# Kernel tuning notes

Hardware: AMD Instinct MI355X
Metric: run time of the kernel (lower is better)

The kernel has to match this reference:

```python
import jax, jax.numpy as jnp
import numpy as np

D = 128
N_ATOMS = 200000
E_ATOMS = 800000
G = 2000            # num molecule graphs = nDrug + nProtein
N_BIG = 7000        # nDrug + nProtein + nSe
E_BIG = 200000
N_EMB = 100001


def _edges(key, n, e):
    # random edges guaranteed to have no self-loops (PyG convs strip/re-add them)
    k1, k2 = jax.random.split(key)
    src = jax.random.randint(k1, (e,), 0, n)
    off = jax.random.randint(k2, (e,), 1, n)
    return jnp.stack([src, (src + off) % n])


def setup_inputs() -> dict:
    key = jax.random.key(0)
    ks = jax.random.split(key, 40)
    s = 0.09  # ~1/sqrt(D) init scale
    nrm = lambda i, shape: jax.random.normal(ks[i], shape, dtype=jnp.float32) * s
    inp = {}
    inp['x_ids'] = jax.random.randint(ks[0], (N_BIG,), 0, N_EMB)
    inp['drugEdges'] = _edges(ks[1], N_BIG, E_BIG)
    inp['seEdges'] = _edges(ks[2], 5000, 1000)  # unused by forward
    inp['drugNodes'] = jax.random.randint(ks[3], (1000,), 0, N_BIG)
    inp['seNodes'] = jax.random.randint(ks[4], (5000,), 0, N_BIG)
    inp['proteinNodes'] = jax.random.randint(ks[5], (1000,), 0, N_EMB)
    inp['proteinWeight'] = jax.random.normal(ks[6], (1000,), dtype=jnp.float32)
    inp['atom_x'] = jax.random.randint(ks[7], (N_ATOMS,), 0, N_EMB)
    inp['atom_edge_index'] = _edges(ks[8], N_ATOMS, E_ATOMS)
    inp['atom_batch'] = jnp.sort(jax.random.randint(ks[9], (N_ATOMS,), 0, G))
    inp['nDrug'] = 1000
    inp['emb'] = jax.random.uniform(ks[10], (N_EMB, D), minval=0.001, maxval=0.3, dtype=jnp.float32)
    for i in range(3):
        inp[f'gatW{i+1}'] = nrm(11 + i, (D, D))
        inp[f'attS{i+1}'] = nrm(14 + i, (D,))
        inp[f'attD{i+1}'] = nrm(17 + i, (D,))
        inp[f'gatB{i+1}'] = nrm(20 + i, (D,))
        inp[f'poolP{i+1}'] = nrm(23 + i, (D,))
    inp['lin1_W'] = nrm(26, (2 * D, D))
    inp['lin1_b'] = nrm(27, (D,))
    inp['gcn1_W'] = nrm(28, (D, D))
    inp['gcn1_b'] = nrm(29, (D,))
    inp['gcn2_W'] = nrm(30, (D, D))
    inp['gcn2_b'] = nrm(31, (D,))
    return inp


def _gat(x, src, dst, n, W, a_s, a_d, b):
    # PyG GATConv, 1 head: h = xW; e_ij = LeakyReLU(a_s.h_j + a_d.h_i);
    # softmax over incoming edges of i (self-loops re-added); out_i = sum_j alpha_ij h_j + b
    h = x @ W
    loops = jnp.arange(n)
    s = jnp.concatenate([src, loops])
    d = jnp.concatenate([dst, loops])
    e = jax.nn.leaky_relu((h @ a_s)[s] + (h @ a_d)[d], 0.2)
    m = jax.ops.segment_max(e, d, num_segments=n)
    ex = jnp.exp(e - m[d])
    z = jax.ops.segment_sum(ex, d, num_segments=n)
    w = ex / z[d]
    return jax.ops.segment_sum(w[:, None] * h[s], d, num_segments=n) + b


def _gcn(x, src, dst, n, W, b):
    loops = jnp.arange(n)
    s = jnp.concatenate([src, loops])
    d = jnp.concatenate([dst, loops])
    deg = jax.ops.segment_sum(jnp.ones(d.shape[0], x.dtype), d, num_segments=n)
    dis = deg ** -0.5
    coef = dis[s] * dis[d]
    return jax.ops.segment_sum(coef[:, None] * (x @ W)[s], d, num_segments=n) + b


def _topk1(x, p):
    # TopKPooling with ratio=1: keep all nodes, gate by tanh of projection score
    score = (x @ p) / jnp.linalg.norm(p)
    return x * jnp.tanh(score)[:, None]


def _gmp_gap(x, batch, g):
    mx = jax.ops.segment_max(x, batch, num_segments=g)
    sm = jax.ops.segment_sum(x, batch, num_segments=g)
    cnt = jax.ops.segment_sum(jnp.ones((x.shape[0], 1), x.dtype), batch, num_segments=g)
    return jnp.concatenate([mx, sm / jnp.maximum(cnt, 1.0)], axis=1)


def reference(x_ids, drugEdges, seEdges, drugNodes, seNodes, proteinNodes, proteinWeight,
              atom_x, atom_edge_index, atom_batch, nDrug, emb,
              gatW1, attS1, attD1, gatB1, poolP1,
              gatW2, attS2, attD2, gatB2, poolP2,
              gatW3, attS3, attD3, gatB3, poolP3,
              lin1_W, lin1_b, gcn1_W, gcn1_b, gcn2_W, gcn2_b):
    na = atom_x.shape[0]
    asrc, adst = atom_edge_index[0], atom_edge_index[1]
    xa = emb[atom_x]                                   # [na, D]
    xa = jax.nn.relu(_gat(xa, asrc, adst, na, gatW1, attS1, attD1, gatB1))
    xa = _topk1(xa, poolP1)
    x1 = _gmp_gap(xa, atom_batch, G)                   # [G, 2D]
    xa = jax.nn.relu(_gat(xa, asrc, adst, na, gatW2, attS2, attD2, gatB2))
    xa = _topk1(xa, poolP2)
    x2 = _gmp_gap(xa, atom_batch, G)
    xa = jax.nn.relu(_gat(xa, asrc, adst, na, gatW3, attS3, attD3, gatB3))
    xa = _topk1(xa, poolP3)
    x3 = _gmp_gap(xa, atom_batch, G)
    xDP = jax.nn.relu((x1 + x2 + x3) @ lin1_W + lin1_b)  # [G, D]
    nProtein = proteinNodes.shape[0]
    xse = emb[x_ids[nDrug + nProtein:]]                # side-effect node embeddings
    xb = jnp.concatenate([xDP, xse], axis=0)           # [N_BIG, D]
    dsrc, ddst = drugEdges[0], drugEdges[1]
    xb = jax.nn.relu(_gcn(xb, dsrc, ddst, N_BIG, gcn1_W, gcn1_b))
    xb = jax.nn.relu(_gcn(xb, dsrc, ddst, N_BIG, gcn2_W, gcn2_b))
    return (xb[drugNodes], xb[seNodes], xb)
```

## Files before the change

kernel.cpp:

```cpp
#include <hip/hip_runtime.h>
#include <cfloat>
#include <cmath>

#define D 128
#define N_ATOMS 200000
#define E_ATOMS 800000
#define G_GROUPS 2000
#define N_BIG 7000
#define E_BIG 200000
#define N_ALL (N_ATOMS + N_BIG)
#define E_ALL (E_ATOMS + E_BIG)

static inline int ceil_div(int a, int b) { return (a + b - 1) / b; }

typedef __attribute__((ext_vector_type(8))) _Float16 f16x8;
typedef __attribute__((ext_vector_type(2))) _Float16 h2_t;
typedef __attribute__((ext_vector_type(4))) float f32x4;

__device__ inline h2_t u2h(unsigned u) { return __builtin_bit_cast(h2_t, u); }
__device__ inline unsigned h2u(h2_t h) { return __builtin_bit_cast(unsigned, h); }
__device__ inline unsigned packh2(float x, float y) {
  h2_t h;
  h[0] = (_Float16)x;
  h[1] = (_Float16)y;
  return h2u(h);
}
__device__ inline float leaky(float e) { return fmaxf(e, 0.2f * e); }
__device__ inline float fast_tanh(float x) {
  float cx = fminf(fmaxf(x, -15.f), 15.f);
  float t = __expf(2.f * cx);
  return (t - 1.f) * __frcp_rn(t + 1.f);
}

__global__ void count_all(const int* __restrict__ adst, const int* __restrict__ ddst, int* __restrict__ deg,
                          int* __restrict__ rank) {
  int i = blockIdx.x * 256 + threadIdx.x;
  if (i < E_ATOMS)
    rank[i] = atomicAdd(&deg[adst[i]], 1);
  else if (i < E_ALL)
    rank[i] = atomicAdd(&deg[N_ATOMS + ddst[i - E_ATOMS]], 1);
}

__global__ void fill_csx(const int* __restrict__ asrc, const int* __restrict__ adst,
                         const int* __restrict__ dsrc, const int* __restrict__ ddst,
                         const int* __restrict__ rpx, const int* __restrict__ rank, int* __restrict__ csx) {
  int i = blockIdx.x * 256 + threadIdx.x;
  if (i < E_ATOMS) {
    csx[rpx[adst[i]] + rank[i]] = asrc[i];
  } else if (i < E_ALL) {
    int k = i - E_ATOMS;
    csx[rpx[N_ATOMS + ddst[k]] + rank[i]] = dsrc[k];
  }
}

__global__ void fill_pad(const int* __restrict__ deg, const int* __restrict__ rpx, int* __restrict__ csx) {
  int d = blockIdx.x * 256 + threadIdx.x;
  if (d >= N_ALL) return;
  int dg = deg[d];
  int b = rpx[d], e = rpx[d + 1];
  int sv = (d < N_ATOMS) ? d : d - N_ATOMS;
  for (int j = b + dg; j < e; ++j) csx[j] = sv;
}

__global__ void post_count(const int* __restrict__ deg, int* __restrict__ cntp, float* __restrict__ dis) {
  int i = blockIdx.x * 256 + threadIdx.x;
  if (i < N_ALL) cntp[i] = (deg[i] + 8) & ~7;
  if (i < N_BIG) dis[i] = 1.f / sqrtf((float)(deg[N_ATOMS + i] + 1));
}

__global__ __launch_bounds__(256) void scan_phase1(const int* __restrict__ in, int* __restrict__ out,
                                                   int* __restrict__ bsums, int n) {
  __shared__ int lds[256];
  int t = threadIdx.x;
  int base = blockIdx.x * 1024;
  int v[4];
  int s = 0;
#pragma unroll
  for (int j = 0; j < 4; ++j) {
    int i = base + t * 4 + j;
    v[j] = (i < n) ? in[i] : 0;
    s += v[j];
  }
  lds[t] = s;
  __syncthreads();
  for (int off = 1; off < 256; off <<= 1) {
    int x = (t >= off) ? lds[t - off] : 0;
    __syncthreads();
    lds[t] += x;
    __syncthreads();
  }
  int excl = lds[t] - s;
  if (t == 255) bsums[blockIdx.x] = lds[255];
  int run = excl;
#pragma unroll
  for (int j = 0; j < 4; ++j) {
    int i = base + t * 4 + j;
    if (i < n) out[i] = run;
    run += v[j];
  }
}

__global__ __launch_bounds__(256) void scan_phase2(int* __restrict__ bsums, int* __restrict__ total_out, int nb) {
  __shared__ int lds[256];
  int t = threadIdx.x;
  int s = (t < nb) ? bsums[t] : 0;
  lds[t] = s;
  __syncthreads();
  for (int off = 1; off < 256; off <<= 1) {
    int x = (t >= off) ? lds[t - off] : 0;
    __syncthreads();
    lds[t] += x;
    __syncthreads();
  }
  if (t < nb) bsums[t] = lds[t] - s;
  if (t == 255) total_out[0] = lds[255];
}

__global__ void scan_phase3(int* __restrict__ out, const int* __restrict__ bsums, int n) {
  int i = blockIdx.x * 256 + threadIdx.x;
  if (i < n) out[i] += bsums[i >> 10];
}

__global__ __launch_bounds__(256) void prep_kernel(const float* __restrict__ W0, const float* __restrict__ W1,
                                                   const float* __restrict__ W2, const float* __restrict__ W3,
                                                   const float* __restrict__ W4, unsigned short* __restrict__ Wsplit,
                                                   const float* __restrict__ p0, const float* __restrict__ p1,
                                                   const float* __restrict__ p2, float* __restrict__ pn) {
  int b = blockIdx.x;
  if (b < 5) {
    const float* W = (b == 0) ? W0 : (b == 1) ? W1 : (b == 2) ? W2 : (b == 3) ? W3 : W4;
    unsigned short* dstH = Wsplit + (size_t)b * 16384;
    int t = threadIdx.x;
    int col = t & 127;
    int half = t >> 7;
#pragma unroll
    for (int kg = 0; kg < 8; ++kg) {
      int k0 = kg * 16 + half * 8;
      f16x8 vh;
#pragma unroll
      for (int j = 0; j < 8; ++j) vh[j] = (_Float16)W[(k0 + j) * 128 + col];
      int byte_off = (col * 256 + k0 * 2) ^ ((col & 7) << 4);
      *(f16x8*)((char*)dstH + byte_off) = vh;
    }
  } else {
    int t = threadIdx.x;
    int g = t >> 6, lane = t & 63;
    if (g < 3) {
      const float* p = (g == 0) ? p0 : (g == 1) ? p1 : p2;
      float2 v = ((const float2*)p)[lane];
      float s = v.x * v.x + v.y * v.y;
#pragma unroll
      for (int off = 32; off; off >>= 1) s += __shfl_xor(s, off);
      if (lane == 0) pn[g] = 1.f / sqrtf(s);
    }
  }
}

__global__ __launch_bounds__(512, 2) void gemm_f16(const unsigned short* __restrict__ A,
                                                   const float* __restrict__ embA, const int* __restrict__ ids,
                                                   const unsigned short* __restrict__ Wsp,
                                                   unsigned short* __restrict__ H, float* __restrict__ hs,
                                                   float* __restrict__ hd, const float* __restrict__ aS,
                                                   const float* __restrict__ aD, int M) {
  __shared__ unsigned short Wl[16384];
  int t = threadIdx.x;
  {
    const uint4* src = (const uint4*)Wsp;
    uint4* dst = (uint4*)Wl;
#pragma unroll
    for (int i = 0; i < 4; ++i) dst[t + i * 512] = src[t + i * 512];
  }
  int wave = t >> 6, lane = t & 63;
  int lr = lane & 15, lq = lane >> 4;
  int row0 = blockIdx.x * 256 + wave * 32;
  f16x8 Af[4][2];
  if (ids) {
    int rid[2];
#pragma unroll
    for (int rt = 0; rt < 2; ++rt) {
      int row = row0 + rt * 16 + lr;
      rid[rt] = (row < M) ? ids[row] : 0;
    }
#pragma unroll
    for (int ks = 0; ks < 4; ++ks)
#pragma unroll
      for (int rt = 0; rt < 2; ++rt) {
        int row = row0 + rt * 16 + lr;
        if (row < M) {
          const float* src = embA + (size_t)rid[rt] * D + ks * 32 + lq * 8;
          float4 v0 = *(const float4*)src;
          float4 v1 = *(const float4*)(src + 4);
          f16x8 a;
          a[0] = (_Float16)v0.x; a[1] = (_Float16)v0.y; a[2] = (_Float16)v0.z; a[3] = (_Float16)v0.w;
          a[4] = (_Float16)v1.x; a[5] = (_Float16)v1.y; a[6] = (_Float16)v1.z; a[7] = (_Float16)v1.w;
          Af[ks][rt] = a;
        } else {
          Af[ks][rt] = (f16x8){0, 0, 0, 0, 0, 0, 0, 0};
        }
      }
  } else {
#pragma unroll
    for (int ks = 0; ks < 4; ++ks)
#pragma unroll
      for (int rt = 0; rt < 2; ++rt) {
        int row = row0 + rt * 16 + lr;
        if (row < M) {
          Af[ks][rt] = *(const f16x8*)(A + (size_t)row * D + ks * 32 + lq * 8);
        } else {
          Af[ks][rt] = (f16x8){0, 0, 0, 0, 0, 0, 0, 0};
        }
      }
  }
  __syncthreads();
  f32x4 acc[2][8];
#pragma unroll
  for (int rt = 0; rt < 2; ++rt)
#pragma unroll
    for (int ct = 0; ct < 8; ++ct) acc[rt][ct] = (f32x4){0.f, 0.f, 0.f, 0.f};

#pragma unroll
  for (int ks = 0; ks < 4; ++ks) {
    int k8 = ks * 32 + lq * 8;
#pragma unroll
    for (int ct = 0; ct < 8; ++ct) {
      int col = ct * 16 + lr;
      int byte_off = (col * 256 + k8 * 2) ^ ((col & 7) << 4);
      f16x8 Bh = *(f16x8*)((char*)Wl + byte_off);
#pragma unroll
      for (int rt = 0; rt < 2; ++rt)
        acc[rt][ct] = __builtin_amdgcn_mfma_f32_16x16x32_f16(Af[ks][rt], Bh, acc[rt][ct], 0, 0, 0);
    }
  }
#pragma unroll
  for (int rt = 0; rt < 2; ++rt)
#pragma unroll
    for (int ct = 0; ct < 8; ++ct) {
      int col = ct * 16 + lr;
#pragma unroll
      for (int i = 0; i < 4; ++i) {
        int row = row0 + rt * 16 + lq * 4 + i;
        if (row < M) {
          _Float16 hv = (_Float16)acc[rt][ct][i];
          H[(size_t)row * D + col] = __builtin_bit_cast(unsigned short, hv);
        }
      }
    }
  if (aS) {
    float sA[8], sD[8];
#pragma unroll
    for (int ct = 0; ct < 8; ++ct) {
      sA[ct] = aS[ct * 16 + lr];
      sD[ct] = aD[ct * 16 + lr];
    }
#pragma unroll
    for (int rt = 0; rt < 2; ++rt)
#pragma unroll
      for (int i = 0; i < 4; ++i) {
        float ps = 0.f, pd = 0.f;
#pragma unroll
        for (int ct = 0; ct < 8; ++ct) {
          ps = fmaf(acc[rt][ct][i], sA[ct], ps);
          pd = fmaf(acc[rt][ct][i], sD[ct], pd);
        }
#pragma unroll
        for (int off = 1; off < 16; off <<= 1) {
          ps += __shfl_xor(ps, off);
          pd += __shfl_xor(pd, off);
        }
        int row = row0 + rt * 16 + lq * 4 + i;
        if (lr == 0 && row < M) {
          hs[row] = ps;
          hd[row] = pd;
        }
      }
  }
}

__global__ void edge_weights(const float* __restrict__ hs, const float* __restrict__ hd,
                             const int* __restrict__ rpx, const int* __restrict__ deg,
                             const int* __restrict__ csx, unsigned* __restrict__ wts,
                             float* __restrict__ invz, int N) {
  int d = blockIdx.x * 256 + threadIdx.x;
  if (d >= N) return;
  int b = rpx[d];
  int cnt = rpx[d + 1] - b;
  int dg = deg[d];
  float hdd = hd[d];
  float z = 0.f;
  for (int j = 0; j < dg; ++j) {
    float w = __expf(leaky(hs[csx[b + j]] + hdd));
    z += w;
    wts[b + j] = packh2(w, w);
  }
  float wself = __expf(leaky(hs[d] + hdd));
  wts[b + dg] = packh2(wself, wself);
  z += wself;
  for (int j = dg + 1; j < cnt; ++j) wts[b + j] = 0;
  invz[d] = 1.f / z;
}

__global__ void gcn_weights(const int* __restrict__ rpx, const int* __restrict__ deg,
                            const int* __restrict__ csx, const float* __restrict__ dis,
                            unsigned* __restrict__ wtsG, int N) {
  int dl = blockIdx.x * 256 + threadIdx.x;
  if (dl >= N) return;
  int d = N_ATOMS + dl;
  int b = rpx[d];
  int cnt = rpx[d + 1] - b;
  int dg = deg[d];
  float dd = dis[dl];
  for (int j = 0; j < dg; ++j) {
    float w = dis[csx[b + j]] * dd;
    wtsG[b + j] = packh2(w, w);
  }
  wtsG[b + dg] = packh2(dd * dd, dd * dd);
  for (int j = dg + 1; j < cnt; ++j) wtsG[b + j] = 0;
}

__global__ __launch_bounds__(256) void gat_gather(const unsigned short* __restrict__ H,
                                                  const int* __restrict__ rpx, const int* __restrict__ csx,
                                                  const unsigned* __restrict__ wts,
                                                  const float* __restrict__ invz, const float* __restrict__ bias,
                                                  const float* __restrict__ poolP, const float* __restrict__ pnL,
                                                  unsigned short* __restrict__ Xout, int N) {
  int wid = (blockIdx.x * 256 + threadIdx.x) >> 6;
  int d = __builtin_amdgcn_readfirstlane(wid);
  if (d >= N) return;
  int lane = threadIdx.x & 63;
  int rb = rpx[d];
  int cnt = rpx[d + 1] - rb;
  const unsigned* H2 = (const unsigned*)H;
  float ax = 0.f, ay = 0.f;
  for (int i = 0; i < cnt; i += 8) {
    int s0 = csx[rb + i + 0], s1 = csx[rb + i + 1], s2 = csx[rb + i + 2], s3 = csx[rb + i + 3];
    int s4 = csx[rb + i + 4], s5 = csx[rb + i + 5], s6 = csx[rb + i + 6], s7 = csx[rb + i + 7];
    unsigned w0 = wts[rb + i + 0], w1 = wts[rb + i + 1], w2 = wts[rb + i + 2], w3 = wts[rb + i + 3];
    unsigned w4 = wts[rb + i + 4], w5 = wts[rb + i + 5], w6 = wts[rb + i + 6], w7 = wts[rb + i + 7];
    unsigned h0 = H2[(size_t)s0 * 64 + lane];
    unsigned h1 = H2[(size_t)s1 * 64 + lane];
    unsigned h2 = H2[(size_t)s2 * 64 + lane];
    unsigned h3 = H2[(size_t)s3 * 64 + lane];
    unsigned h4 = H2[(size_t)s4 * 64 + lane];
    unsigned h5 = H2[(size_t)s5 * 64 + lane];
    unsigned h6 = H2[(size_t)s6 * 64 + lane];
    unsigned h7 = H2[(size_t)s7 * 64 + lane];
    h2_t a2 = u2h(w0) * u2h(h0);
    a2 += u2h(w1) * u2h(h1);
    a2 += u2h(w2) * u2h(h2);
    a2 += u2h(w3) * u2h(h3);
    h2_t b2h = u2h(w4) * u2h(h4);
    b2h += u2h(w5) * u2h(h5);
    b2h += u2h(w6) * u2h(h6);
    b2h += u2h(w7) * u2h(h7);
    a2 += b2h;
    ax += (float)a2[0];
    ay += (float)a2[1];
  }
  float iz = invz[d];
  float2 b2 = ((const float2*)bias)[lane];
  ax = fmaxf(fmaf(ax, iz, b2.x), 0.f);
  ay = fmaxf(fmaf(ay, iz, b2.y), 0.f);
  float2 p2 = ((const float2*)poolP)[lane];
  float dot = ax * p2.x + ay * p2.y;
#pragma unroll
  for (int off = 32; off; off >>= 1) dot += __shfl_xor(dot, off);
  float sc = fast_tanh(dot * pnL[0]);
  ((unsigned*)Xout)[(size_t)d * 64 + lane] = packh2(ax * sc, ay * sc);
}

__global__ __launch_bounds__(256) void gcn_gather(const unsigned short* __restrict__ Y,
                                                  const int* __restrict__ rpx, const int* __restrict__ csx,
                                                  const unsigned* __restrict__ wtsG, const float* __restrict__ b,
                                                  unsigned short* __restrict__ outB, float* __restrict__ outF,
                                                  int N) {
  int wid = (blockIdx.x * 256 + threadIdx.x) >> 6;
  int dl = __builtin_amdgcn_readfirstlane(wid);
  if (dl >= N) return;
  int lane = threadIdx.x & 63;
  int rb = rpx[N_ATOMS + dl];
  int cnt = rpx[N_ATOMS + dl + 1] - rb;
  const unsigned* Y2 = (const unsigned*)Y;
  float ax = 0.f, ay = 0.f;
  for (int i = 0; i < cnt; i += 8) {
    int s0 = csx[rb + i + 0], s1 = csx[rb + i + 1], s2 = csx[rb + i + 2], s3 = csx[rb + i + 3];
    int s4 = csx[rb + i + 4], s5 = csx[rb + i + 5], s6 = csx[rb + i + 6], s7 = csx[rb + i + 7];
    unsigned w0 = wtsG[rb + i + 0], w1 = wtsG[rb + i + 1], w2 = wtsG[rb + i + 2], w3 = wtsG[rb + i + 3];
    unsigned w4 = wtsG[rb + i + 4], w5 = wtsG[rb + i + 5], w6 = wtsG[rb + i + 6], w7 = wtsG[rb + i + 7];
    unsigned h0 = Y2[(size_t)s0 * 64 + lane];
    unsigned h1 = Y2[(size_t)s1 * 64 + lane];
    unsigned h2 = Y2[(size_t)s2 * 64 + lane];
    unsigned h3 = Y2[(size_t)s3 * 64 + lane];
    unsigned h4 = Y2[(size_t)s4 * 64 + lane];
    unsigned h5 = Y2[(size_t)s5 * 64 + lane];
    unsigned h6 = Y2[(size_t)s6 * 64 + lane];
    unsigned h7 = Y2[(size_t)s7 * 64 + lane];
    h2_t a2 = u2h(w0) * u2h(h0);
    a2 += u2h(w1) * u2h(h1);
    a2 += u2h(w2) * u2h(h2);
    a2 += u2h(w3) * u2h(h3);
    h2_t b2h = u2h(w4) * u2h(h4);
    b2h += u2h(w5) * u2h(h5);
    b2h += u2h(w6) * u2h(h6);
    b2h += u2h(w7) * u2h(h7);
    a2 += b2h;
    ax += (float)a2[0];
    ay += (float)a2[1];
  }
  float2 b2 = ((const float2*)b)[lane];
  float ox = fmaxf(ax + b2.x, 0.f);
  float oy = fmaxf(ay + b2.y, 0.f);
  if (outF)
    ((float2*)outF)[(size_t)dl * 64 + lane] = make_float2(ox, oy);
  else
    ((unsigned*)outB)[(size_t)dl * 64 + lane] = packh2(ox, oy);
}

__global__ void group_bounds(const int* __restrict__ batch, int* __restrict__ gs, int* __restrict__ ge, int n) {
  int i = blockIdx.x * 256 + threadIdx.x;
  if (i >= n) return;
  int b = batch[i];
  if (i == 0 || batch[i - 1] != b) gs[b] = i;
  if (i == n - 1 || batch[i + 1] != b) ge[b] = i + 1;
}

__global__ __launch_bounds__(256) void pool_kernel(const unsigned short* __restrict__ X,
                                                   const int* __restrict__ gs, const int* __restrict__ ge,
                                                   float* __restrict__ x123) {
  __shared__ float2 mxs[4][64];
  __shared__ float2 sms[4][64];
  int g = blockIdx.x;
  int wv = threadIdx.x >> 6;
  int p = threadIdx.x & 63;
  int beg = gs[g], end = ge[g];
  int cnt = end - beg;
  const unsigned* X2 = (const unsigned*)X;
  float mx0 = -FLT_MAX, mx1 = -FLT_MAX, sm0 = 0.f, sm1 = 0.f;
  for (int i = beg + wv; i < end; i += 4) {
    h2_t v = u2h(X2[(size_t)i * 64 + p]);
    float a = (float)v[0], b = (float)v[1];
    mx0 = fmaxf(mx0, a);
    mx1 = fmaxf(mx1, b);
    sm0 += a;
    sm1 += b;
  }
  mxs[wv][p] = make_float2(mx0, mx1);
  sms[wv][p] = make_float2(sm0, sm1);
  __syncthreads();
  if (threadIdx.x < 64 && cnt > 0) {
#pragma unroll
    for (int k = 1; k < 4; ++k) {
      float2 m2 = mxs[k][p], s2 = sms[k][p];
      mx0 = fmaxf(mx0, m2.x);
      mx1 = fmaxf(mx1, m2.y);
      sm0 += s2.x;
      sm1 += s2.y;
    }
    float inv = 1.f / (float)cnt;
    float* xg = x123 + (size_t)g * 256;
    xg[2 * p] += mx0;
    xg[2 * p + 1] += mx1;
    xg[128 + 2 * p] += sm0 * inv;
    xg[128 + 2 * p + 1] += sm1 * inv;
  }
}

__global__ __launch_bounds__(128) void lin1_kernel(const float* __restrict__ x123, const float* __restrict__ W,
                                                   const float* __restrict__ b, unsigned short* __restrict__ xb) {
  __shared__ float row[256];
  int g = blockIdx.x;
  int c = threadIdx.x;
  row[c] = x123[(size_t)g * 256 + c];
  row[c + 128] = x123[(size_t)g * 256 + 128 + c];
  __syncthreads();
  float acc = b[c];
#pragma unroll 8
  for (int k = 0; k < 256; ++k) acc = fmaf(row[k], W[k * 128 + c], acc);
  _Float16 hv = (_Float16)fmaxf(acc, 0.f);
  xb[(size_t)g * D + c] = __builtin_bit_cast(unsigned short, hv);
}

__global__ void xse_kernel(const float* __restrict__ emb, const int* __restrict__ x_ids,
                           const int* __restrict__ nDrugPtr, int nProtein, unsigned short* __restrict__ xb) {
  int idx = blockIdx.x * 256 + threadIdx.x;
  int r = idx >> 6, lane = idx & 63;
  int off = nDrugPtr[0] + nProtein;
  int id = x_ids[off + r];
  float2 v = ((const float2*)(emb + (size_t)id * D))[lane];
  ((unsigned*)xb)[(size_t)(G_GROUPS + r) * 64 + lane] = packh2(v.x, v.y);
}

__global__ void out_gather(const float* __restrict__ xb, const int* __restrict__ dn, const int* __restrict__ sn,
                           float* __restrict__ out) {
  int idx = blockIdx.x * 256 + threadIdx.x;
  int r = idx >> 6, lane = idx & 63;
  int s = (r < 1000) ? dn[r] : (r < 6000) ? sn[r - 1000] : (r - 6000);
  ((float2*)out)[(size_t)idx] = ((const float2*)(xb + (size_t)s * D))[lane];
}

extern "C" void kernel_launch(void* const* d_in, const int* in_sizes, int n_in, void* d_out, int out_size,
                              void* d_ws, size_t ws_size, hipStream_t stream) {
  const int* x_ids = (const int*)d_in[0];
  const int* drugE = (const int*)d_in[1];
  const int* drugNodes = (const int*)d_in[3];
  const int* seNodes = (const int*)d_in[4];
  int nProtein = in_sizes[5];
  const int* atom_x = (const int*)d_in[7];
  const int* atomE = (const int*)d_in[8];
  const int* atom_batch = (const int*)d_in[9];
  const int* nDrugPtr = (const int*)d_in[10];
  const float* emb = (const float*)d_in[11];
  const float* gatW[3] = {(const float*)d_in[12], (const float*)d_in[17], (const float*)d_in[22]};
  const float* attS[3] = {(const float*)d_in[13], (const float*)d_in[18], (const float*)d_in[23]};
  const float* attD[3] = {(const float*)d_in[14], (const float*)d_in[19], (const float*)d_in[24]};
  const float* gatB[3] = {(const float*)d_in[15], (const float*)d_in[20], (const float*)d_in[25]};
  const float* poolP[3] = {(const float*)d_in[16], (const float*)d_in[21], (const float*)d_in[26]};
  const float* lin1_W = (const float*)d_in[27];
  const float* lin1_b = (const float*)d_in[28];
  const float* gcn1_W = (const float*)d_in[29];
  const float* gcn1_b = (const float*)d_in[30];
  const float* gcn2_W = (const float*)d_in[31];
  const float* gcn2_b = (const float*)d_in[32];
  float* out = (float*)d_out;
  (void)n_in; (void)out_size; (void)ws_size;

  const int MAXX = E_ALL + 8 * N_ALL;

  char* ws = (char*)d_ws;
  size_t off = 0;
  auto alloc = [&](size_t bytes) -> char* {
    char* p = ws + off;
    off += (bytes + 255) & ~(size_t)255;
    return p;
  };
  unsigned short* bufA = (unsigned short*)alloc((size_t)N_ATOMS * D * 2);
  unsigned short* bufB = (unsigned short*)alloc((size_t)N_ATOMS * D * 2);
  float* hs = (float*)alloc((size_t)N_ATOMS * 4);
  float* hd = (float*)alloc((size_t)N_ATOMS * 4);
  int* csx = (int*)alloc((size_t)MAXX * 4);
  unsigned* wts = (unsigned*)alloc((size_t)MAXX * 4);
  unsigned* wtsG = (unsigned*)alloc((size_t)MAXX * 4);
  int* rank = (int*)alloc((size_t)E_ALL * 4);
  float* invz = (float*)alloc((size_t)N_ATOMS * 4);
  float* x123 = (float*)alloc((size_t)G_GROUPS * 256 * 4);
  unsigned short* xb1 = (unsigned short*)alloc((size_t)N_BIG * D * 2);
  unsigned short* xb2 = (unsigned short*)alloc((size_t)N_BIG * D * 2);
  float* xbF = (float*)alloc((size_t)N_BIG * D * 4);
  unsigned short* Wsplit = (unsigned short*)alloc((size_t)5 * 16384 * 2);
  int* rpx = (int*)alloc((size_t)(N_ALL + 1) * 4);
  int* deg = (int*)alloc((size_t)N_ALL * 4);
  int* cntp = (int*)alloc((size_t)N_ALL * 4);
  float* disB = (float*)alloc((size_t)N_BIG * 4);
  int* gs = (int*)alloc((size_t)G_GROUPS * 4);
  int* ge = (int*)alloc((size_t)G_GROUPS * 4);
  int* bsums = (int*)alloc(256 * 4);
  float* pn = (float*)alloc(256);

  const int* asrc = atomE;
  const int* adst = atomE + E_ATOMS;
  const int* dsrc = drugE;
  const int* ddst = drugE + E_BIG;

  prep_kernel<<<6, 256, 0, stream>>>(gatW[0], gatW[1], gatW[2], gcn1_W, gcn2_W, Wsplit, poolP[0], poolP[1],
                                     poolP[2], pn);

  hipMemsetAsync(deg, 0, (size_t)N_ALL * 4, stream);
  count_all<<<ceil_div(E_ALL, 256), 256, 0, stream>>>(adst, ddst, deg, rank);
  post_count<<<ceil_div(N_ALL, 256), 256, 0, stream>>>(deg, cntp, disB);
  scan_phase1<<<ceil_div(N_ALL, 1024), 256, 0, stream>>>(cntp, rpx, bsums, N_ALL);
  scan_phase2<<<1, 256, 0, stream>>>(bsums, rpx + N_ALL, ceil_div(N_ALL, 1024));
  scan_phase3<<<ceil_div(N_ALL, 256), 256, 0, stream>>>(rpx, bsums, N_ALL);
  fill_csx<<<ceil_div(E_ALL, 256), 256, 0, stream>>>(asrc, adst, dsrc, ddst, rpx, rank, csx);
  fill_pad<<<ceil_div(N_ALL, 256), 256, 0, stream>>>(deg, rpx, csx);
  gcn_weights<<<ceil_div(N_BIG, 256), 256, 0, stream>>>(rpx, deg, csx, disB, wtsG, N_BIG);

  hipMemsetAsync(gs, 0, (size_t)G_GROUPS * 4, stream);
  hipMemsetAsync(ge, 0, (size_t)G_GROUPS * 4, stream);
  group_bounds<<<ceil_div(N_ATOMS, 256), 256, 0, stream>>>(atom_batch, gs, ge, N_ATOMS);

  hipMemsetAsync(x123, 0, (size_t)G_GROUPS * 256 * 4, stream);

  for (int L = 0; L < 3; ++L) {
    gemm_f16<<<ceil_div(N_ATOMS, 256), 512, 0, stream>>>(bufA, emb, (L == 0) ? atom_x : nullptr,
                                                         Wsplit + (size_t)L * 16384, bufB, hs, hd, attS[L],
                                                         attD[L], N_ATOMS);
    edge_weights<<<ceil_div(N_ATOMS, 256), 256, 0, stream>>>(hs, hd, rpx, deg, csx, wts, invz, N_ATOMS);
    gat_gather<<<N_ATOMS * 64 / 256, 256, 0, stream>>>(bufB, rpx, csx, wts, invz, gatB[L], poolP[L], pn + L,
                                                       bufA, N_ATOMS);
    pool_kernel<<<G_GROUPS, 256, 0, stream>>>(bufA, gs, ge, x123);
  }

  lin1_kernel<<<G_GROUPS, 128, 0, stream>>>(x123, lin1_W, lin1_b, xb1);
  xse_kernel<<<(N_BIG - G_GROUPS) * 64 / 256, 256, 0, stream>>>(emb, x_ids, nDrugPtr, nProtein, xb1);

  gemm_f16<<<ceil_div(N_BIG, 256), 512, 0, stream>>>(xb1, nullptr, nullptr, Wsplit + (size_t)3 * 16384, bufB,
                                                     nullptr, nullptr, nullptr, nullptr, N_BIG);
  gcn_gather<<<N_BIG * 64 / 256, 256, 0, stream>>>(bufB, rpx, csx, wtsG, gcn1_b, xb2, nullptr, N_BIG);
  gemm_f16<<<ceil_div(N_BIG, 256), 512, 0, stream>>>(xb2, nullptr, nullptr, Wsplit + (size_t)4 * 16384, bufB,
                                                     nullptr, nullptr, nullptr, nullptr, N_BIG);
  gcn_gather<<<N_BIG * 64 / 256, 256, 0, stream>>>(bufB, rpx, csx, wtsG, gcn2_b, nullptr, xbF, N_BIG);

  out_gather<<<13000 * 64 / 256, 256, 0, stream>>>(xbF, drugNodes, seNodes, out);
}
```

Measured before the change: 496.6 us.

## Pre-normalize GAT edge weights and gather two nodes per wavefront

edge_weights now divides each attention weight by the softmax denominator before packing it to fp16. This removes the invz buffer and the per-node scaling in the gather. gat_gather is remapped so each 64-lane wave handles two destination nodes, one per 32-lane half, with each lane loading 8 bytes (4 features). The intent is to halve the wave count and widen the per-lane loads. In exchange, a half-wave idles when its node has fewer edges than its partner, and each wave reads both nodes' index and weight lists, so rpx and the weight buffer get padding to cover reads past the last node.

```diff
diff --git a/kernel.cpp b/kernel.cpp
--- a/kernel.cpp
+++ b/kernel.cpp
@@ -278,25 +278,29 @@
 
 __global__ void edge_weights(const float* __restrict__ hs, const float* __restrict__ hd,
                              const int* __restrict__ rpx, const int* __restrict__ deg,
-                             const int* __restrict__ csx, unsigned* __restrict__ wts,
-                             float* __restrict__ invz, int N) {
+                             const int* __restrict__ csx, unsigned* __restrict__ wts, int N) {
   int d = blockIdx.x * 256 + threadIdx.x;
   if (d >= N) return;
   int b = rpx[d];
   int cnt = rpx[d + 1] - b;
   int dg = deg[d];
   float hdd = hd[d];
+  float* wf = (float*)wts;
   float z = 0.f;
   for (int j = 0; j < dg; ++j) {
     float w = __expf(leaky(hs[csx[b + j]] + hdd));
     z += w;
-    wts[b + j] = packh2(w, w);
+    wf[b + j] = w;
   }
   float wself = __expf(leaky(hs[d] + hdd));
-  wts[b + dg] = packh2(wself, wself);
+  wf[b + dg] = wself;
   z += wself;
+  float iz = 1.f / z;
+  for (int j = 0; j <= dg; ++j) {
+    float wn = wf[b + j] * iz;
+    wts[b + j] = packh2(wn, wn);
+  }
   for (int j = dg + 1; j < cnt; ++j) wts[b + j] = 0;
-  invz[d] = 1.f / z;
 }
 
 __global__ void gcn_weights(const int* __restrict__ rpx, const int* __restrict__ deg,
@@ -320,52 +324,65 @@
 __global__ __launch_bounds__(256) void gat_gather(const unsigned short* __restrict__ H,
                                                   const int* __restrict__ rpx, const int* __restrict__ csx,
                                                   const unsigned* __restrict__ wts,
-                                                  const float* __restrict__ invz, const float* __restrict__ bias,
+                                                  const float* __restrict__ bias,
                                                   const float* __restrict__ poolP, const float* __restrict__ pnL,
                                                   unsigned short* __restrict__ Xout, int N) {
   int wid = (blockIdx.x * 256 + threadIdx.x) >> 6;
-  int d = __builtin_amdgcn_readfirstlane(wid);
-  if (d >= N) return;
+  int d0 = __builtin_amdgcn_readfirstlane(wid << 1);
+  if (d0 >= N) return;
   int lane = threadIdx.x & 63;
-  int rb = rpx[d];
-  int cnt = rpx[d + 1] - rb;
-  const unsigned* H2 = (const unsigned*)H;
-  float ax = 0.f, ay = 0.f;
-  for (int i = 0; i < cnt; i += 8) {
-    int s0 = csx[rb + i + 0], s1 = csx[rb + i + 1], s2 = csx[rb + i + 2], s3 = csx[rb + i + 3];
-    int s4 = csx[rb + i + 4], s5 = csx[rb + i + 5], s6 = csx[rb + i + 6], s7 = csx[rb + i + 7];
-    unsigned w0 = wts[rb + i + 0], w1 = wts[rb + i + 1], w2 = wts[rb + i + 2], w3 = wts[rb + i + 3];
-    unsigned w4 = wts[rb + i + 4], w5 = wts[rb + i + 5], w6 = wts[rb + i + 6], w7 = wts[rb + i + 7];
-    unsigned h0 = H2[(size_t)s0 * 64 + lane];
-    unsigned h1 = H2[(size_t)s1 * 64 + lane];
-    unsigned h2 = H2[(size_t)s2 * 64 + lane];
-    unsigned h3 = H2[(size_t)s3 * 64 + lane];
-    unsigned h4 = H2[(size_t)s4 * 64 + lane];
-    unsigned h5 = H2[(size_t)s5 * 64 + lane];
-    unsigned h6 = H2[(size_t)s6 * 64 + lane];
-    unsigned h7 = H2[(size_t)s7 * 64 + lane];
-    h2_t a2 = u2h(w0) * u2h(h0);
-    a2 += u2h(w1) * u2h(h1);
-    a2 += u2h(w2) * u2h(h2);
-    a2 += u2h(w3) * u2h(h3);
-    h2_t b2h = u2h(w4) * u2h(h4);
-    b2h += u2h(w5) * u2h(h5);
-    b2h += u2h(w6) * u2h(h6);
-    b2h += u2h(w7) * u2h(h7);
-    a2 += b2h;
-    ax += (float)a2[0];
-    ay += (float)a2[1];
-  }
-  float iz = invz[d];
-  float2 b2 = ((const float2*)bias)[lane];
-  ax = fmaxf(fmaf(ax, iz, b2.x), 0.f);
-  ay = fmaxf(fmaf(ay, iz, b2.y), 0.f);
-  float2 p2 = ((const float2*)poolP)[lane];
-  float dot = ax * p2.x + ay * p2.y;
-#pragma unroll
-  for (int off = 32; off; off >>= 1) dot += __shfl_xor(dot, off);
+  int half = lane >> 5;
+  int hl = lane & 31;
+  int rb0 = rpx[d0];
+  int rb1 = rpx[d0 + 1];
+  int rb2 = rpx[d0 + 2];
+  int cnt0 = rb1 - rb0;
+  int cnt1 = rb2 - rb1;
+  int rb_h = half ? rb1 : rb0;
+  int cnt_h = half ? cnt1 : cnt0;
+  const uint2* H2 = (const uint2*)H;
+  float a0 = 0.f, a1 = 0.f, a2 = 0.f, a3 = 0.f;
+  for (int i = 0; i < cnt_h; i += 8) {
+    int ib = __builtin_amdgcn_readfirstlane(i);
+    int sA[8], sB[8];
+    unsigned wA[8], wB[8];
+#pragma unroll
+    for (int j = 0; j < 8; ++j) {
+      sA[j] = csx[rb0 + ib + j];
+      sB[j] = csx[rb1 + ib + j];
+      wA[j] = wts[rb0 + ib + j];
+      wB[j] = wts[rb1 + ib + j];
+    }
+    h2_t acc0 = (h2_t){(_Float16)0.f, (_Float16)0.f};
+    h2_t acc1 = acc0;
+#pragma unroll
+    for (int j = 0; j < 8; ++j) {
+      int sj = half ? sB[j] : sA[j];
+      unsigned wj = half ? wB[j] : wA[j];
+      uint2 hv = H2[(size_t)sj * 32 + hl];
+      h2_t wh = u2h(wj);
+      acc0 += wh * u2h(hv.x);
+      acc1 += wh * u2h(hv.y);
+    }
+    a0 += (float)acc0[0];
+    a1 += (float)acc0[1];
+    a2 += (float)acc1[0];
+    a3 += (float)acc1[1];
+  }
+  float4 b4 = ((const float4*)bias)[hl];
+  a0 = fmaxf(a0 + b4.x, 0.f);
+  a1 = fmaxf(a1 + b4.y, 0.f);
+  a2 = fmaxf(a2 + b4.z, 0.f);
+  a3 = fmaxf(a3 + b4.w, 0.f);
+  float4 p4 = ((const float4*)poolP)[hl];
+  float dot = a0 * p4.x + a1 * p4.y + a2 * p4.z + a3 * p4.w;
+#pragma unroll
+  for (int off = 16; off; off >>= 1) dot += __shfl_xor(dot, off);
   float sc = fast_tanh(dot * pnL[0]);
-  ((unsigned*)Xout)[(size_t)d * 64 + lane] = packh2(ax * sc, ay * sc);
+  uint2 o;
+  o.x = packh2(a0 * sc, a1 * sc);
+  o.y = packh2(a2 * sc, a3 * sc);
+  ((uint2*)Xout)[(size_t)(d0 + half) * 32 + hl] = o;
 }
 
 __global__ __launch_bounds__(256) void gcn_gather(const unsigned short* __restrict__ Y,
@@ -523,7 +540,7 @@
   float* out = (float*)d_out;
   (void)n_in; (void)out_size; (void)ws_size;
 
-  const int MAXX = E_ALL + 8 * N_ALL;
+  const int MAXX = E_ALL + 8 * N_ALL + 64;
 
   char* ws = (char*)d_ws;
   size_t off = 0;
@@ -540,13 +557,12 @@
   unsigned* wts = (unsigned*)alloc((size_t)MAXX * 4);
   unsigned* wtsG = (unsigned*)alloc((size_t)MAXX * 4);
   int* rank = (int*)alloc((size_t)E_ALL * 4);
-  float* invz = (float*)alloc((size_t)N_ATOMS * 4);
   float* x123 = (float*)alloc((size_t)G_GROUPS * 256 * 4);
   unsigned short* xb1 = (unsigned short*)alloc((size_t)N_BIG * D * 2);
   unsigned short* xb2 = (unsigned short*)alloc((size_t)N_BIG * D * 2);
   float* xbF = (float*)alloc((size_t)N_BIG * D * 4);
   unsigned short* Wsplit = (unsigned short*)alloc((size_t)5 * 16384 * 2);
-  int* rpx = (int*)alloc((size_t)(N_ALL + 1) * 4);
+  int* rpx = (int*)alloc((size_t)(N_ALL + 2) * 4);
   int* deg = (int*)alloc((size_t)N_ALL * 4);
   int* cntp = (int*)alloc((size_t)N_ALL * 4);
   float* disB = (float*)alloc((size_t)N_BIG * 4);
@@ -583,9 +599,9 @@
     gemm_f16<<<ceil_div(N_ATOMS, 256), 512, 0, stream>>>(bufA, emb, (L == 0) ? atom_x : nullptr,
                                                          Wsplit + (size_t)L * 16384, bufB, hs, hd, attS[L],
                                                          attD[L], N_ATOMS);
-    edge_weights<<<ceil_div(N_ATOMS, 256), 256, 0, stream>>>(hs, hd, rpx, deg, csx, wts, invz, N_ATOMS);
-    gat_gather<<<N_ATOMS * 64 / 256, 256, 0, stream>>>(bufB, rpx, csx, wts, invz, gatB[L], poolP[L], pn + L,
-                                                       bufA, N_ATOMS);
+    edge_weights<<<ceil_div(N_ATOMS, 256), 256, 0, stream>>>(hs, hd, rpx, deg, csx, wts, N_ATOMS);
+    gat_gather<<<ceil_div(N_ATOMS / 2 * 64, 256), 256, 0, stream>>>(bufB, rpx, csx, wts, gatB[L], poolP[L],
+                                                                    pn + L, bufA, N_ATOMS);
     pool_kernel<<<G_GROUPS, 256, 0, stream>>>(bufA, gs, ge, x123);
   }
 
```

After: 471.7 us. -5.0%, faster.
